# Kernel tuning notes

Hardware: AMD Instinct MI355X
Metric: run time of the kernel (lower is better)

## Reference

```python
import jax, jax.numpy as jnp
import numpy as np

K = 3      # kernel size (fixed by 18 = 2*K*K offset channels)
PAD = 1
EPS = 1e-5 # BatchNorm eps


def setup_inputs() -> dict:
    key = jax.random.key(0)
    ks = jax.random.split(key, 4)
    B, Cin, Cout, H, W = 8, 64, 64, 96, 96
    x = jax.random.normal(ks[0], (B, Cin, H, W), jnp.float32)
    # small offset-conv weights so predicted offsets stay within a few pixels
    w_off = jax.random.normal(ks[1], (2 * K * K, Cin, K, K), jnp.float32) * 0.02
    b_off = jnp.zeros((2 * K * K,), jnp.float32)
    w_def = jax.random.normal(ks[2], (Cout, Cin, K, K), jnp.float32) * (1.0 / np.sqrt(Cin * K * K))
    b_def = jnp.zeros((Cout,), jnp.float32)
    gamma = jnp.ones((Cout,), jnp.float32)
    beta = jnp.zeros((Cout,), jnp.float32)
    return dict(x=x, w_off=w_off, b_off=b_off, w_def=w_def, b_def=b_def, gamma=gamma, beta=beta)


def _deform_sample(x, offset):
    """Bilinear-sample x at deformed kernel tap locations.
    x: (B,C,H,W); offset: (B,2*K*K,H,W) with (dy,dx) pairs per tap, row-major.
    Returns (B,C,K*K,H,W). Out-of-bounds samples are zero (torchvision semantics).
    """
    B, C, H, W = x.shape
    off = offset.reshape(B, K * K, 2, H, W)
    dy, dx = off[:, :, 0], off[:, :, 1]              # (B,9,H,W)
    ky = (jnp.arange(K * K) // K).astype(x.dtype)    # tap row index
    kx = (jnp.arange(K * K) % K).astype(x.dtype)     # tap col index
    base_y = jnp.arange(H, dtype=x.dtype)[:, None] - PAD   # (H,1)
    base_x = jnp.arange(W, dtype=x.dtype)[None, :] - PAD   # (1,W)
    py = dy + ky[None, :, None, None] + base_y[None, None]  # (B,9,H,W)
    px = dx + kx[None, :, None, None] + base_x[None, None]
    y0 = jnp.floor(py)
    x0 = jnp.floor(px)
    wy1 = py - y0
    wx1 = px - x0
    wy0 = 1.0 - wy1
    wx0 = 1.0 - wx1
    xflat = x.reshape(B, C, H * W)
    acc = jnp.zeros((B, C, K * K * H * W), x.dtype)
    corners = [(y0, x0, wy0 * wx0), (y0, x0 + 1.0, wy0 * wx1),
               (y0 + 1.0, x0, wy1 * wx0), (y0 + 1.0, x0 + 1.0, wy1 * wx1)]
    for yc, xc, wc in corners:
        valid = (yc >= 0) & (yc <= H - 1) & (xc >= 0) & (xc <= W - 1)
        iy = jnp.clip(yc, 0, H - 1).astype(jnp.int32)
        ix = jnp.clip(xc, 0, W - 1).astype(jnp.int32)
        idx = (iy * W + ix).reshape(B, 1, K * K * H * W)
        v = jnp.take_along_axis(xflat, idx, axis=2)          # (B,C,9HW) gather
        w = jnp.where(valid, wc, 0.0).reshape(B, 1, K * K * H * W)
        acc = acc + v * w
    return acc.reshape(B, C, K * K, H, W)


def reference(x, w_off, b_off, w_def, b_def, gamma, beta):
    # 1) offset-predicting conv
    offset = jax.lax.conv_general_dilated(
        x, w_off, window_strides=(1, 1), padding=((PAD, PAD), (PAD, PAD)),
        dimension_numbers=("NCHW", "OIHW", "NCHW")) + b_off[None, :, None, None]
    # 2) deformable conv: bilinear gather then per-pixel contraction over (C, taps)
    sampled = _deform_sample(x, offset)                      # (B,C,9,H,W)
    Cout = w_def.shape[0]
    y = jnp.einsum("bckhw,ock->bohw", sampled, w_def.reshape(Cout, -1, K * K))
    y = y + b_def[None, :, None, None]
    # 3) BatchNorm2d (training mode: batch statistics) + ReLU
    mean = y.mean(axis=(0, 2, 3))
    var = y.var(axis=(0, 2, 3))
    y = (y - mean[None, :, None, None]) * jax.lax.rsqrt(var[None, :, None, None] + EPS)
    y = gamma[None, :, None, None] * y + beta[None, :, None, None]
    return jax.nn.relu(y)
```

## Files before the change

### kernel.cpp

```cpp
#include <hip/hip_runtime.h>
#include <hip/hip_bf16.h>
#include <stdint.h>

static constexpr int NBATCH = 8;
static constexpr int Cin  = 64;
static constexpr int Cout = 64;
static constexpr int H = 96, W = 96;
static constexpr int HW   = H * W;
static constexpr int NPIX = NBATCH * HW;
static constexpr int NBLK = NPIX / 64;
static constexpr int BLK_PER_BATCH = HW / 64;
static constexpr float EPS = 1e-5f;

typedef short  bf16x8 __attribute__((ext_vector_type(8)));
typedef float  f32x4  __attribute__((ext_vector_type(4)));

__device__ inline uint16_t f2bf(float f) {
    __hip_bfloat16 h = __float2bfloat16(f);
    return *reinterpret_cast<uint16_t*>(&h);
}
__device__ inline float bf2f(uint16_t u) {
    union { uint32_t i; float f; } z;
    z.i = ((uint32_t)u) << 16;
    return z.f;
}
__device__ inline void gld_lds16(const void* g, void* l) {
    __builtin_amdgcn_global_load_lds(
        (const __attribute__((address_space(1))) void*)g,
        (__attribute__((address_space(3))) void*)l, 16, 0, 0);
}

__global__ void repack(const float* __restrict__ w_off,
                       const float* __restrict__ w_def,
                       uint16_t* __restrict__ woffPack,
                       uint16_t* __restrict__ wdefPack,
                       float* __restrict__ zeropage) {
    int t0 = blockIdx.x * blockDim.x + threadIdx.x;
    int stride = gridDim.x * blockDim.x;
    if (t0 < 64) zeropage[t0] = 0.f;
    for (int i = t0; i < 72 * 32 * 8; i += stride) {
        int e = i & 7;
        int n = (i >> 3) & 31;
        int sg = i >> 8;
        int k = sg * 8 + e;
        int tap = k >> 6, c = k & 63;
        woffPack[i] = (n < 18) ? f2bf(w_off[(n * Cin + c) * 9 + tap]) : (uint16_t)0;
    }
    for (int i = t0; i < 72 * 64 * 8; i += stride) {
        int e = i & 7;
        int n = (i >> 3) & 63;
        int sg = i >> 9;
        int k = sg * 8 + e;
        int tap = k >> 6, c = k & 63;
        wdefPack[i] = f2bf(w_def[(n * Cin + c) * 9 + tap]);
    }
}

__global__ __launch_bounds__(256) void transpose_x(const float* __restrict__ x,
                                                   uint16_t* __restrict__ xT) {
    int t = blockIdx.x * 256 + threadIdx.x;
    int pix  = t >> 1;
    int half = t & 1;
    int b = pix / HW, rem = pix % HW;
    const float* xb = x + (size_t)(b * Cin) * HW + rem + (size_t)(half * 32) * HW;
    uint16_t* o = xT + (size_t)pix * 64 + half * 32;
#pragma unroll
    for (int cg = 0; cg < 4; ++cg) {
        bf16x8 v;
#pragma unroll
        for (int e = 0; e < 8; ++e) v[e] = (short)f2bf(xb[(cg * 8 + e) * HW]);
        *reinterpret_cast<bf16x8*>(o + cg * 8) = v;
    }
}

__global__ __launch_bounds__(512, 4) void fused_deform(
        const uint16_t* __restrict__ xT,
        const uint16_t* __restrict__ woffPack,
        const uint16_t* __restrict__ wdefPack,
        const float* __restrict__ b_off,
        const float* __restrict__ zeropage,
        float* __restrict__ y,
        float* __restrict__ partial) {
    __shared__ __attribute__((aligned(16))) char smem[73728];
    __shared__ float offs[64 * 18];
    __shared__ float s_red[128];
    short* As   = (short*)smem;
    float* osum = (float*)smem;
    float* red  = (float*)smem;

    int tid  = threadIdx.x;
    int lane = tid & 63;
    int wv   = tid >> 6;
    int l15  = lane & 15;
    int lg   = lane >> 4;

    int wgid  = (blockIdx.x & 7) * BLK_PER_BATCH + (blockIdx.x >> 3);
    int gpix0 = wgid * 64;
    int b     = gpix0 / HW;
    int rem0  = gpix0 % HW;
    const uint16_t* xTb = xT + (size_t)b * HW * 64;

    int pr   = (wv << 3) + (lane >> 3);
    int e8   = lane & 7;
    int slot = e8 ^ (pr & 7);
    int remP = rem0 + pr;
    int hP   = remP / W, wP = remP % W;

    {
        const uint16_t* gsrc = xTb + slot * 8;
        char* ldsbase = (char*)As + (size_t)wv * 1024;
#pragma unroll
        for (int tap = 0; tap < 9; ++tap) {
            int yy = hP + tap / 3 - 1;
            int xx = wP + tap % 3 - 1;
            bool ok = (yy >= 0) && (yy < H) && (xx >= 0) && (xx < W);
            const void* g = ok ? (const void*)(gsrc + (yy * W + xx) * 64)
                               : (const void*)zeropage;
            gld_lds16(g, ldsbase + tap * 8192);
        }
    }
    __syncthreads();

    {
        int wj = wv & 1;
        int kq = wv >> 1;
        int sbeg = (kq < 2) ? kq * 5 : 2 + kq * 4;
        int send = (kq < 2) ? sbeg + 5 : sbeg + 4;
        f32x4 oacc[4];
#pragma unroll
        for (int m = 0; m < 4; ++m) oacc[m] = (f32x4){0.f, 0.f, 0.f, 0.f};
        for (int s = sbeg; s < send; ++s) {
            int sg = s * 4 + lg;
            bf16x8 bb = *reinterpret_cast<const bf16x8*>(
                woffPack + (sg * 32 + wj * 16 + l15) * 8);
#pragma unroll
            for (int m = 0; m < 4; ++m) {
                bf16x8 a = *reinterpret_cast<const bf16x8*>(
                    &As[(((sg >> 3) * 64 + m * 16 + l15) * 8 + ((sg & 7) ^ (l15 & 7))) * 8]);
                oacc[m] = __builtin_amdgcn_mfma_f32_16x16x32_bf16(a, bb, oacc[m], 0, 0, 0);
            }
        }
        __syncthreads();
#pragma unroll
        for (int m = 0; m < 4; ++m)
#pragma unroll
            for (int r = 0; r < 4; ++r)
                osum[(kq * 64 + m * 16 + lg * 4 + r) * 34 + wj * 16 + l15] = oacc[m][r];
        __syncthreads();
        for (int i = tid; i < 64 * 18; i += 512) {
            int rr = i / 18, o = i - rr * 18;
            offs[i] = osum[rr * 34 + o] + osum[(64 + rr) * 34 + o]
                    + osum[(128 + rr) * 34 + o] + osum[(192 + rr) * 34 + o] + b_off[o];
        }
        if (tid < 128) s_red[tid] = 0.f;
        __syncthreads();
    }

    {
        float hm1 = (float)(hP - 1), wm1 = (float)(wP - 1);
        float w00a, w01a, w10a, w11a; int i00a, i01a, i10a, i11a;
        {
            int t = e8;
            int ty = (t * 11) >> 5;
            int tx = t - 3 * ty;
            float dy = offs[pr * 18 + 2 * t];
            float dx = offs[pr * 18 + 2 * t + 1];
            float py = dy + (float)ty + hm1;
            float px = dx + (float)tx + wm1;
            float y0f = floorf(py), x0f = floorf(px);
            float wy1 = py - y0f, wx1 = px - x0f;
            float wy0 = 1.f - wy1, wx0 = 1.f - wx1;
            int iy0 = (int)y0f, ix0 = (int)x0f;
            int iy1 = iy0 + 1,  ix1 = ix0 + 1;
            bool vy0 = (iy0 >= 0) && (iy0 < H), vy1 = (iy1 >= 0) && (iy1 < H);
            bool vx0 = (ix0 >= 0) && (ix0 < W), vx1 = (ix1 >= 0) && (ix1 < W);
            w00a = (vy0 && vx0) ? wy0 * wx0 : 0.f;
            w01a = (vy0 && vx1) ? wy0 * wx1 : 0.f;
            w10a = (vy1 && vx0) ? wy1 * wx0 : 0.f;
            w11a = (vy1 && vx1) ? wy1 * wx1 : 0.f;
            int cy0 = min(max(iy0, 0), H - 1), cy1 = min(max(iy1, 0), H - 1);
            int cx0 = min(max(ix0, 0), W - 1), cx1 = min(max(ix1, 0), W - 1);
            i00a = cy0 * W + cx0; i01a = cy0 * W + cx1;
            i10a = cy1 * W + cx0; i11a = cy1 * W + cx1;
        }
        float w00b, w01b, w10b, w11b; int i00b, i01b, i10b, i11b;
        {
            float dy = offs[pr * 18 + 16];
            float dx = offs[pr * 18 + 17];
            float py = dy + 2.f + hm1;
            float px = dx + 2.f + wm1;
            float y0f = floorf(py), x0f = floorf(px);
            float wy1 = py - y0f, wx1 = px - x0f;
            float wy0 = 1.f - wy1, wx0 = 1.f - wx1;
            int iy0 = (int)y0f, ix0 = (int)x0f;
            int iy1 = iy0 + 1,  ix1 = ix0 + 1;
            bool vy0 = (iy0 >= 0) && (iy0 < H), vy1 = (iy1 >= 0) && (iy1 < H);
            bool vx0 = (ix0 >= 0) && (ix0 < W), vx1 = (ix1 >= 0) && (ix1 < W);
            w00b = (vy0 && vx0) ? wy0 * wx0 : 0.f;
            w01b = (vy0 && vx1) ? wy0 * wx1 : 0.f;
            w10b = (vy1 && vx0) ? wy1 * wx0 : 0.f;
            w11b = (vy1 && vx1) ? wy1 * wx1 : 0.f;
            int cy0 = min(max(iy0, 0), H - 1), cy1 = min(max(iy1, 0), H - 1);
            int cx0 = min(max(ix0, 0), W - 1), cx1 = min(max(ix1, 0), W - 1);
            i00b = cy0 * W + cx0; i01b = cy0 * W + cx1;
            i10b = cy1 * W + cx0; i11b = cy1 * W + cx1;
        }

        const uint16_t* basep = xTb + e8 * 8;
        int lanebase = lane & 56;
#pragma unroll
        for (int tap = 0; tap < 9; ++tap) {
            float w00, w01, w10, w11; int i00, i01, i10, i11;
            if (tap < 8) {
                int src = lanebase + tap;
                w00 = __shfl(w00a, src); w01 = __shfl(w01a, src);
                w10 = __shfl(w10a, src); w11 = __shfl(w11a, src);
                i00 = __shfl(i00a, src); i01 = __shfl(i01a, src);
                i10 = __shfl(i10a, src); i11 = __shfl(i11a, src);
            } else {
                w00 = w00b; w01 = w01b; w10 = w10b; w11 = w11b;
                i00 = i00b; i01 = i01b; i10 = i10b; i11 = i11b;
            }
            bf16x8 v00 = *reinterpret_cast<const bf16x8*>(basep + i00 * 64);
            bf16x8 v01 = *reinterpret_cast<const bf16x8*>(basep + i01 * 64);
            bf16x8 v10 = *reinterpret_cast<const bf16x8*>(basep + i10 * 64);
            bf16x8 v11 = *reinterpret_cast<const bf16x8*>(basep + i11 * 64);
            bf16x8 outv;
#pragma unroll
            for (int e = 0; e < 8; ++e) {
                float s = w00 * bf2f((uint16_t)v00[e]) + w01 * bf2f((uint16_t)v01[e])
                        + w10 * bf2f((uint16_t)v10[e]) + w11 * bf2f((uint16_t)v11[e]);
                outv[e] = (short)f2bf(s);
            }
            *reinterpret_cast<bf16x8*>(&As[((tap * 64 + pr) * 8 + slot) * 8]) = outv;
        }
    }
    __syncthreads();

    {
        int nf = wv & 3;
        int kh = wv >> 2;
        f32x4 acc[4];
#pragma unroll
        for (int m = 0; m < 4; ++m) acc[m] = (f32x4){0.f, 0.f, 0.f, 0.f};
#pragma unroll
        for (int s = 0; s < 9; ++s) {
            int sg = (kh * 9 + s) * 4 + lg;
            bf16x8 bb = *reinterpret_cast<const bf16x8*>(
                wdefPack + (sg * 64 + nf * 16 + l15) * 8);
#pragma unroll
            for (int m = 0; m < 4; ++m) {
                bf16x8 a = *reinterpret_cast<const bf16x8*>(
                    &As[(((sg >> 3) * 64 + m * 16 + l15) * 8 + ((sg & 7) ^ (l15 & 7))) * 8]);
                acc[m] = __builtin_amdgcn_mfma_f32_16x16x32_bf16(a, bb, acc[m], 0, 0, 0);
            }
        }
        __syncthreads();
#pragma unroll
        for (int m = 0; m < 4; ++m)
#pragma unroll
            for (int r = 0; r < 4; ++r)
                red[(kh * 64 + m * 16 + lg * 4 + r) * 66 + nf * 16 + l15] = acc[m][r];
        __syncthreads();

        int c  = lane;
        int rg = wv;
        f32x4 v0, v1;
        float s = 0.f, q = 0.f;
#pragma unroll
        for (int k2 = 0; k2 < 8; ++k2) {
            int r = rg * 8 + k2;
            float v = red[r * 66 + c] + red[(64 + r) * 66 + c];
            if (k2 < 4) v0[k2] = v; else v1[k2 - 4] = v;
            s += v; q += v * v;
        }
        float* yp = y + ((size_t)b * Cout + c) * HW + rem0 + rg * 8;
        *reinterpret_cast<f32x4*>(yp)     = v0;
        *reinterpret_cast<f32x4*>(yp + 4) = v1;
        atomicAdd(&s_red[c], s);
        atomicAdd(&s_red[64 + c], q);
    }
    __syncthreads();
    if (tid < 128) partial[(size_t)wgid * 128 + tid] = s_red[tid];
}

__global__ __launch_bounds__(256) void bn_reduce1(const float* __restrict__ partial,
                                                  float* __restrict__ partial2) {
    __shared__ float red[256];
    int ch = threadIdx.x & 127;
    int g  = threadIdx.x >> 7;
    float s = 0.f;
#pragma unroll
    for (int r = 0; r < 8; ++r)
        s += partial[(size_t)(blockIdx.x * 16 + g * 8 + r) * 128 + ch];
    red[threadIdx.x] = s;
    __syncthreads();
    if (g == 0)
        partial2[(size_t)blockIdx.x * 128 + ch] = red[ch] + red[128 + ch];
}

__global__ void bn_stats2(const float* __restrict__ partial2,
                          const float* __restrict__ gamma,
                          const float* __restrict__ beta,
                          float* __restrict__ stats) {
    __shared__ float red[256];
    int ch = threadIdx.x & 127;
    int g  = threadIdx.x >> 7;
    float s = 0.f;
    for (int i = 0; i < 36; ++i)
        s += partial2[(size_t)(g * 36 + i) * 128 + ch];
    red[threadIdx.x] = s;
    __syncthreads();
    if (threadIdx.x < 64) {
        int c = threadIdx.x;
        float sum = red[c] + red[128 + c];
        float sq  = red[64 + c] + red[192 + c];
        float mean = sum / (float)NPIX;
        float var  = sq / (float)NPIX - mean * mean;
        float v    = var + EPS;
        float inv  = rsqrtf(v);
        inv = inv * (1.5f - 0.5f * v * inv * inv);
        float sc = gamma[c] * inv;
        stats[c]      = sc;
        stats[64 + c] = beta[c] - mean * sc;
    }
}

__global__ __launch_bounds__(256) void bn_apply(float* __restrict__ y,
                                                const float* __restrict__ stats) {
    int t = blockIdx.x * blockDim.x + threadIdx.x;
    int e = t * 4;
    int ch = (e / HW) % Cout;
    float sc = stats[ch];
    float sh = stats[64 + ch];
    float4 v = *reinterpret_cast<float4*>(y + e);
    v.x = fmaxf(v.x * sc + sh, 0.f);
    v.y = fmaxf(v.y * sc + sh, 0.f);
    v.z = fmaxf(v.z * sc + sh, 0.f);
    v.w = fmaxf(v.w * sc + sh, 0.f);
    *reinterpret_cast<float4*>(y + e) = v;
}

extern "C" void kernel_launch(void* const* d_in, const int* in_sizes, int n_in,
                              void* d_out, int out_size, void* d_ws, size_t ws_size,
                              hipStream_t stream) {
    const float* x     = (const float*)d_in[0];
    const float* w_off = (const float*)d_in[1];
    const float* b_off = (const float*)d_in[2];
    const float* w_def = (const float*)d_in[3];
    const float* gamma = (const float*)d_in[5];
    const float* beta  = (const float*)d_in[6];
    float* out = (float*)d_out;
    char*  ws  = (char*)d_ws;

    uint16_t* xT       = (uint16_t*)ws;
    uint16_t* woffPack = (uint16_t*)(ws + 9437184);
    uint16_t* wdefPack = (uint16_t*)(ws + 9474048);
    float*    partial  = (float*)(ws + 9547776);
    float*    partial2 = (float*)(ws + 10137600);
    float*    stats    = (float*)(ws + 10174464);
    float*    zeropage = (float*)(ws + 10174976);

    repack<<<64, 256, 0, stream>>>(w_off, w_def, woffPack, wdefPack, zeropage);
    transpose_x<<<NPIX * 2 / 256, 256, 0, stream>>>(x, xT);
    fused_deform<<<NBLK, 512, 0, stream>>>(xT, woffPack, wdefPack, b_off,
                                           zeropage, out, partial);
    bn_reduce1<<<72, 256, 0, stream>>>(partial, partial2);
    bn_stats2<<<1, 256, 0, stream>>>(partial2, gamma, beta, stats);
    bn_apply<<<(NPIX * Cout / 4) / 256, 256, 0, stream>>>(out, stats);
}
```

Before: 67.08 us.

## Shrink LDS footprint by splitting deform taps and reading offset-conv inputs from global

The offset-conv stage now loads its A operands straight from global memory with bounds masking, instead of staging all 9 im2col taps in LDS through global_load_lds. The deformable sampling and MFMA contraction run in two phases (taps 0-3, then 4-8) that reuse a smaller LDS buffer. This cuts shared memory from 72KB to 40KB so the launch bounds can request more resident blocks. The two BN reduction kernels are also merged into a single 1024-thread kernel to save a launch. In exchange, the offset conv makes redundant uncoalesced global/L2 reads, and the extra phase adds barriers.

```diff
diff --git a/kernel.cpp b/kernel.cpp
--- a/kernel.cpp
+++ b/kernel.cpp
@@ -24,20 +24,13 @@
     z.i = ((uint32_t)u) << 16;
     return z.f;
 }
-__device__ inline void gld_lds16(const void* g, void* l) {
-    __builtin_amdgcn_global_load_lds(
-        (const __attribute__((address_space(1))) void*)g,
-        (__attribute__((address_space(3))) void*)l, 16, 0, 0);
-}
 
 __global__ void repack(const float* __restrict__ w_off,
                        const float* __restrict__ w_def,
                        uint16_t* __restrict__ woffPack,
-                       uint16_t* __restrict__ wdefPack,
-                       float* __restrict__ zeropage) {
+                       uint16_t* __restrict__ wdefPack) {
     int t0 = blockIdx.x * blockDim.x + threadIdx.x;
     int stride = gridDim.x * blockDim.x;
-    if (t0 < 64) zeropage[t0] = 0.f;
     for (int i = t0; i < 72 * 32 * 8; i += stride) {
         int e = i & 7;
         int n = (i >> 3) & 31;
@@ -73,15 +66,14 @@
     }
 }
 
-__global__ __launch_bounds__(512, 4) void fused_deform(
+__global__ __launch_bounds__(512, 6) void fused_deform(
         const uint16_t* __restrict__ xT,
         const uint16_t* __restrict__ woffPack,
         const uint16_t* __restrict__ wdefPack,
         const float* __restrict__ b_off,
-        const float* __restrict__ zeropage,
         float* __restrict__ y,
         float* __restrict__ partial) {
-    __shared__ __attribute__((aligned(16))) char smem[73728];
+    __shared__ __attribute__((aligned(16))) char smem[40960];
     __shared__ float offs[64 * 18];
     __shared__ float s_red[128];
     short* As   = (short*)smem;
@@ -106,41 +98,40 @@
     int remP = rem0 + pr;
     int hP   = remP / W, wP = remP % W;
 
-    {
-        const uint16_t* gsrc = xTb + slot * 8;
-        char* ldsbase = (char*)As + (size_t)wv * 1024;
-#pragma unroll
-        for (int tap = 0; tap < 9; ++tap) {
-            int yy = hP + tap / 3 - 1;
-            int xx = wP + tap % 3 - 1;
-            bool ok = (yy >= 0) && (yy < H) && (xx >= 0) && (xx < W);
-            const void* g = ok ? (const void*)(gsrc + (yy * W + xx) * 64)
-                               : (const void*)zeropage;
-            gld_lds16(g, ldsbase + tap * 8192);
-        }
-    }
-    __syncthreads();
+    if (tid < 128) s_red[tid] = 0.f;
 
     {
         int wj = wv & 1;
         int kq = wv >> 1;
         int sbeg = (kq < 2) ? kq * 5 : 2 + kq * 4;
         int send = (kq < 2) ? sbeg + 5 : sbeg + 4;
+        int rm0 = rem0 + l15,      h0_ = rm0 / W, w0_ = rm0 % W;
+        int rm1 = rem0 + 16 + l15, h1_ = rm1 / W, w1_ = rm1 % W;
+        int rm2 = rem0 + 32 + l15, h2_ = rm2 / W, w2_ = rm2 % W;
+        int rm3 = rem0 + 48 + l15, h3_ = rm3 / W, w3_ = rm3 % W;
         f32x4 oacc[4];
 #pragma unroll
         for (int m = 0; m < 4; ++m) oacc[m] = (f32x4){0.f, 0.f, 0.f, 0.f};
         for (int s = sbeg; s < send; ++s) {
-            int sg = s * 4 + lg;
+            int sg  = s * 4 + lg;
+            int tap = s >> 1;
+            int ty  = tap / 3 - 1, tx = tap % 3 - 1;
+            int ch  = (s & 1) * 4 + lg;
             bf16x8 bb = *reinterpret_cast<const bf16x8*>(
                 woffPack + (sg * 32 + wj * 16 + l15) * 8);
 #pragma unroll
             for (int m = 0; m < 4; ++m) {
+                int hh = (m == 0 ? h0_ : m == 1 ? h1_ : m == 2 ? h2_ : h3_) + ty;
+                int ww = (m == 0 ? w0_ : m == 1 ? w1_ : m == 2 ? w2_ : w3_) + tx;
+                bool ok = (hh >= 0) && (hh < H) && (ww >= 0) && (ww < W);
+                int cy = min(max(hh, 0), H - 1);
+                int cx = min(max(ww, 0), W - 1);
                 bf16x8 a = *reinterpret_cast<const bf16x8*>(
-                    &As[(((sg >> 3) * 64 + m * 16 + l15) * 8 + ((sg & 7) ^ (l15 & 7))) * 8]);
+                    xTb + (cy * W + cx) * 64 + ch * 8);
+                if (!ok) a = (bf16x8){0, 0, 0, 0, 0, 0, 0, 0};
                 oacc[m] = __builtin_amdgcn_mfma_f32_16x16x32_bf16(a, bb, oacc[m], 0, 0, 0);
             }
         }
-        __syncthreads();
 #pragma unroll
         for (int m = 0; m < 4; ++m)
 #pragma unroll
@@ -152,117 +143,148 @@
             offs[i] = osum[rr * 34 + o] + osum[(64 + rr) * 34 + o]
                     + osum[(128 + rr) * 34 + o] + osum[(192 + rr) * 34 + o] + b_off[o];
         }
-        if (tid < 128) s_red[tid] = 0.f;
         __syncthreads();
     }
 
+    float hm1 = (float)(hP - 1), wm1 = (float)(wP - 1);
+    float w00a, w01a, w10a, w11a; int i00a, i01a, i10a, i11a;
     {
-        float hm1 = (float)(hP - 1), wm1 = (float)(wP - 1);
-        float w00a, w01a, w10a, w11a; int i00a, i01a, i10a, i11a;
-        {
-            int t = e8;
-            int ty = (t * 11) >> 5;
-            int tx = t - 3 * ty;
-            float dy = offs[pr * 18 + 2 * t];
-            float dx = offs[pr * 18 + 2 * t + 1];
-            float py = dy + (float)ty + hm1;
-            float px = dx + (float)tx + wm1;
-            float y0f = floorf(py), x0f = floorf(px);
-            float wy1 = py - y0f, wx1 = px - x0f;
-            float wy0 = 1.f - wy1, wx0 = 1.f - wx1;
-            int iy0 = (int)y0f, ix0 = (int)x0f;
-            int iy1 = iy0 + 1,  ix1 = ix0 + 1;
-            bool vy0 = (iy0 >= 0) && (iy0 < H), vy1 = (iy1 >= 0) && (iy1 < H);
-            bool vx0 = (ix0 >= 0) && (ix0 < W), vx1 = (ix1 >= 0) && (ix1 < W);
-            w00a = (vy0 && vx0) ? wy0 * wx0 : 0.f;
-            w01a = (vy0 && vx1) ? wy0 * wx1 : 0.f;
-            w10a = (vy1 && vx0) ? wy1 * wx0 : 0.f;
-            w11a = (vy1 && vx1) ? wy1 * wx1 : 0.f;
-            int cy0 = min(max(iy0, 0), H - 1), cy1 = min(max(iy1, 0), H - 1);
-            int cx0 = min(max(ix0, 0), W - 1), cx1 = min(max(ix1, 0), W - 1);
-            i00a = cy0 * W + cx0; i01a = cy0 * W + cx1;
-            i10a = cy1 * W + cx0; i11a = cy1 * W + cx1;
-        }
-        float w00b, w01b, w10b, w11b; int i00b, i01b, i10b, i11b;
-        {
-            float dy = offs[pr * 18 + 16];
-            float dx = offs[pr * 18 + 17];
-            float py = dy + 2.f + hm1;
-            float px = dx + 2.f + wm1;
-            float y0f = floorf(py), x0f = floorf(px);
-            float wy1 = py - y0f, wx1 = px - x0f;
-            float wy0 = 1.f - wy1, wx0 = 1.f - wx1;
-            int iy0 = (int)y0f, ix0 = (int)x0f;
-            int iy1 = iy0 + 1,  ix1 = ix0 + 1;
-            bool vy0 = (iy0 >= 0) && (iy0 < H), vy1 = (iy1 >= 0) && (iy1 < H);
-            bool vx0 = (ix0 >= 0) && (ix0 < W), vx1 = (ix1 >= 0) && (ix1 < W);
-            w00b = (vy0 && vx0) ? wy0 * wx0 : 0.f;
-            w01b = (vy0 && vx1) ? wy0 * wx1 : 0.f;
-            w10b = (vy1 && vx0) ? wy1 * wx0 : 0.f;
-            w11b = (vy1 && vx1) ? wy1 * wx1 : 0.f;
-            int cy0 = min(max(iy0, 0), H - 1), cy1 = min(max(iy1, 0), H - 1);
-            int cx0 = min(max(ix0, 0), W - 1), cx1 = min(max(ix1, 0), W - 1);
-            i00b = cy0 * W + cx0; i01b = cy0 * W + cx1;
-            i10b = cy1 * W + cx0; i11b = cy1 * W + cx1;
-        }
-
-        const uint16_t* basep = xTb + e8 * 8;
-        int lanebase = lane & 56;
-#pragma unroll
-        for (int tap = 0; tap < 9; ++tap) {
-            float w00, w01, w10, w11; int i00, i01, i10, i11;
-            if (tap < 8) {
-                int src = lanebase + tap;
-                w00 = __shfl(w00a, src); w01 = __shfl(w01a, src);
-                w10 = __shfl(w10a, src); w11 = __shfl(w11a, src);
-                i00 = __shfl(i00a, src); i01 = __shfl(i01a, src);
-                i10 = __shfl(i10a, src); i11 = __shfl(i11a, src);
-            } else {
-                w00 = w00b; w01 = w01b; w10 = w10b; w11 = w11b;
-                i00 = i00b; i01 = i01b; i10 = i10b; i11 = i11b;
-            }
-            bf16x8 v00 = *reinterpret_cast<const bf16x8*>(basep + i00 * 64);
-            bf16x8 v01 = *reinterpret_cast<const bf16x8*>(basep + i01 * 64);
-            bf16x8 v10 = *reinterpret_cast<const bf16x8*>(basep + i10 * 64);
-            bf16x8 v11 = *reinterpret_cast<const bf16x8*>(basep + i11 * 64);
-            bf16x8 outv;
-#pragma unroll
-            for (int e = 0; e < 8; ++e) {
-                float s = w00 * bf2f((uint16_t)v00[e]) + w01 * bf2f((uint16_t)v01[e])
-                        + w10 * bf2f((uint16_t)v10[e]) + w11 * bf2f((uint16_t)v11[e]);
-                outv[e] = (short)f2bf(s);
-            }
-            *reinterpret_cast<bf16x8*>(&As[((tap * 64 + pr) * 8 + slot) * 8]) = outv;
-        }
-    }
-    __syncthreads();
-
+        int t = e8;
+        int ty = (t * 11) >> 5;
+        int tx = t - 3 * ty;
+        float dy = offs[pr * 18 + 2 * t];
+        float dx = offs[pr * 18 + 2 * t + 1];
+        float py = dy + (float)ty + hm1;
+        float px = dx + (float)tx + wm1;
+        float y0f = floorf(py), x0f = floorf(px);
+        float wy1 = py - y0f, wx1 = px - x0f;
+        float wy0 = 1.f - wy1, wx0 = 1.f - wx1;
+        int iy0 = (int)y0f, ix0 = (int)x0f;
+        int iy1 = iy0 + 1,  ix1 = ix0 + 1;
+        bool vy0 = (iy0 >= 0) && (iy0 < H), vy1 = (iy1 >= 0) && (iy1 < H);
+        bool vx0 = (ix0 >= 0) && (ix0 < W), vx1 = (ix1 >= 0) && (ix1 < W);
+        w00a = (vy0 && vx0) ? wy0 * wx0 : 0.f;
+        w01a = (vy0 && vx1) ? wy0 * wx1 : 0.f;
+        w10a = (vy1 && vx0) ? wy1 * wx0 : 0.f;
+        w11a = (vy1 && vx1) ? wy1 * wx1 : 0.f;
+        int cy0 = min(max(iy0, 0), H - 1), cy1 = min(max(iy1, 0), H - 1);
+        int cx0 = min(max(ix0, 0), W - 1), cx1 = min(max(ix1, 0), W - 1);
+        i00a = cy0 * W + cx0; i01a = cy0 * W + cx1;
+        i10a = cy1 * W + cx0; i11a = cy1 * W + cx1;
+    }
+    float w00b, w01b, w10b, w11b; int i00b, i01b, i10b, i11b;
     {
-        int nf = wv & 3;
-        int kh = wv >> 2;
-        f32x4 acc[4];
-#pragma unroll
-        for (int m = 0; m < 4; ++m) acc[m] = (f32x4){0.f, 0.f, 0.f, 0.f};
-#pragma unroll
-        for (int s = 0; s < 9; ++s) {
-            int sg = (kh * 9 + s) * 4 + lg;
-            bf16x8 bb = *reinterpret_cast<const bf16x8*>(
-                wdefPack + (sg * 64 + nf * 16 + l15) * 8);
-#pragma unroll
-            for (int m = 0; m < 4; ++m) {
-                bf16x8 a = *reinterpret_cast<const bf16x8*>(
-                    &As[(((sg >> 3) * 64 + m * 16 + l15) * 8 + ((sg & 7) ^ (l15 & 7))) * 8]);
-                acc[m] = __builtin_amdgcn_mfma_f32_16x16x32_bf16(a, bb, acc[m], 0, 0, 0);
-            }
-        }
-        __syncthreads();
-#pragma unroll
-        for (int m = 0; m < 4; ++m)
-#pragma unroll
-            for (int r = 0; r < 4; ++r)
-                red[(kh * 64 + m * 16 + lg * 4 + r) * 66 + nf * 16 + l15] = acc[m][r];
-        __syncthreads();
-
+        float dy = offs[pr * 18 + 16];
+        float dx = offs[pr * 18 + 17];
+        float py = dy + 2.f + hm1;
+        float px = dx + 2.f + wm1;
+        float y0f = floorf(py), x0f = floorf(px);
+        float wy1 = py - y0f, wx1 = px - x0f;
+        float wy0 = 1.f - wy1, wx0 = 1.f - wx1;
+        int iy0 = (int)y0f, ix0 = (int)x0f;
+        int iy1 = iy0 + 1,  ix1 = ix0 + 1;
+        bool vy0 = (iy0 >= 0) && (iy0 < H), vy1 = (iy1 >= 0) && (iy1 < H);
+        bool vx0 = (ix0 >= 0) && (ix0 < W), vx1 = (ix1 >= 0) && (ix1 < W);
+        w00b = (vy0 && vx0) ? wy0 * wx0 : 0.f;
+        w01b = (vy0 && vx1) ? wy0 * wx1 : 0.f;
+        w10b = (vy1 && vx0) ? wy1 * wx0 : 0.f;
+        w11b = (vy1 && vx1) ? wy1 * wx1 : 0.f;
+        int cy0 = min(max(iy0, 0), H - 1), cy1 = min(max(iy1, 0), H - 1);
+        int cx0 = min(max(ix0, 0), W - 1), cx1 = min(max(ix1, 0), W - 1);
+        i00b = cy0 * W + cx0; i01b = cy0 * W + cx1;
+        i10b = cy1 * W + cx0; i11b = cy1 * W + cx1;
+    }
+    const uint16_t* basep = xTb + e8 * 8;
+    int lanebase = lane & 56;
+    int nf = wv & 3;
+    int kh = wv >> 2;
+    f32x4 acc[4];
+#pragma unroll
+    for (int m = 0; m < 4; ++m) acc[m] = (f32x4){0.f, 0.f, 0.f, 0.f};
+
+#pragma unroll
+    for (int tap = 0; tap < 4; ++tap) {
+        int src = lanebase + tap;
+        float w00 = __shfl(w00a, src), w01 = __shfl(w01a, src);
+        float w10 = __shfl(w10a, src), w11 = __shfl(w11a, src);
+        int i00 = __shfl(i00a, src), i01 = __shfl(i01a, src);
+        int i10 = __shfl(i10a, src), i11 = __shfl(i11a, src);
+        bf16x8 v00 = *reinterpret_cast<const bf16x8*>(basep + i00 * 64);
+        bf16x8 v01 = *reinterpret_cast<const bf16x8*>(basep + i01 * 64);
+        bf16x8 v10 = *reinterpret_cast<const bf16x8*>(basep + i10 * 64);
+        bf16x8 v11 = *reinterpret_cast<const bf16x8*>(basep + i11 * 64);
+        bf16x8 outv;
+#pragma unroll
+        for (int e = 0; e < 8; ++e) {
+            float s = w00 * bf2f((uint16_t)v00[e]) + w01 * bf2f((uint16_t)v01[e])
+                    + w10 * bf2f((uint16_t)v10[e]) + w11 * bf2f((uint16_t)v11[e]);
+            outv[e] = (short)f2bf(s);
+        }
+        *reinterpret_cast<bf16x8*>(&As[((tap * 64 + pr) * 8 + slot) * 8]) = outv;
+    }
+    __syncthreads();
+#pragma unroll
+    for (int i = 0; i < 4; ++i) {
+        int sg = kh * 16 + i * 4 + lg;
+        bf16x8 bb = *reinterpret_cast<const bf16x8*>(
+            wdefPack + (sg * 64 + nf * 16 + l15) * 8);
+#pragma unroll
+        for (int m = 0; m < 4; ++m) {
+            bf16x8 a = *reinterpret_cast<const bf16x8*>(
+                &As[(((sg >> 3) * 64 + m * 16 + l15) * 8 + ((sg & 7) ^ (l15 & 7))) * 8]);
+            acc[m] = __builtin_amdgcn_mfma_f32_16x16x32_bf16(a, bb, acc[m], 0, 0, 0);
+        }
+    }
+    __syncthreads();
+
+#pragma unroll
+    for (int tap = 4; tap < 9; ++tap) {
+        float w00, w01, w10, w11; int i00, i01, i10, i11;
+        if (tap < 8) {
+            int src = lanebase + tap;
+            w00 = __shfl(w00a, src); w01 = __shfl(w01a, src);
+            w10 = __shfl(w10a, src); w11 = __shfl(w11a, src);
+            i00 = __shfl(i00a, src); i01 = __shfl(i01a, src);
+            i10 = __shfl(i10a, src); i11 = __shfl(i11a, src);
+        } else {
+            w00 = w00b; w01 = w01b; w10 = w10b; w11 = w11b;
+            i00 = i00b; i01 = i01b; i10 = i10b; i11 = i11b;
+        }
+        bf16x8 v00 = *reinterpret_cast<const bf16x8*>(basep + i00 * 64);
+        bf16x8 v01 = *reinterpret_cast<const bf16x8*>(basep + i01 * 64);
+        bf16x8 v10 = *reinterpret_cast<const bf16x8*>(basep + i10 * 64);
+        bf16x8 v11 = *reinterpret_cast<const bf16x8*>(basep + i11 * 64);
+        bf16x8 outv;
+#pragma unroll
+        for (int e = 0; e < 8; ++e) {
+            float s = w00 * bf2f((uint16_t)v00[e]) + w01 * bf2f((uint16_t)v01[e])
+                    + w10 * bf2f((uint16_t)v10[e]) + w11 * bf2f((uint16_t)v11[e]);
+            outv[e] = (short)f2bf(s);
+        }
+        *reinterpret_cast<bf16x8*>(&As[(((tap - 4) * 64 + pr) * 8 + slot) * 8]) = outv;
+    }
+    __syncthreads();
+#pragma unroll
+    for (int i = 0; i < 5; ++i) {
+        int sgl = kh * 20 + i * 4 + lg;
+        bf16x8 bb = *reinterpret_cast<const bf16x8*>(
+            wdefPack + ((32 + sgl) * 64 + nf * 16 + l15) * 8);
+#pragma unroll
+        for (int m = 0; m < 4; ++m) {
+            bf16x8 a = *reinterpret_cast<const bf16x8*>(
+                &As[(((sgl >> 3) * 64 + m * 16 + l15) * 8 + ((sgl & 7) ^ (l15 & 7))) * 8]);
+            acc[m] = __builtin_amdgcn_mfma_f32_16x16x32_bf16(a, bb, acc[m], 0, 0, 0);
+        }
+    }
+    __syncthreads();
+
+#pragma unroll
+    for (int m = 0; m < 4; ++m)
+#pragma unroll
+        for (int r = 0; r < 4; ++r)
+            red[(kh * 64 + m * 16 + lg * 4 + r) * 66 + nf * 16 + l15] = acc[m][r];
+    __syncthreads();
+    {
         int c  = lane;
         int rg = wv;
         f32x4 v0, v1;
@@ -284,45 +306,34 @@
     if (tid < 128) partial[(size_t)wgid * 128 + tid] = s_red[tid];
 }
 
-__global__ __launch_bounds__(256) void bn_reduce1(const float* __restrict__ partial,
-                                                  float* __restrict__ partial2) {
-    __shared__ float red[256];
-    int ch = threadIdx.x & 127;
-    int g  = threadIdx.x >> 7;
+__global__ __launch_bounds__(1024) void bn_stats(const float* __restrict__ partial,
+                                                 const float* __restrict__ gamma,
+                                                 const float* __restrict__ beta,
+                                                 float* __restrict__ stats) {
+    __shared__ float red[1024];
+    int t = threadIdx.x, ch = t & 127, part = t >> 7;
     float s = 0.f;
-#pragma unroll
-    for (int r = 0; r < 8; ++r)
-        s += partial[(size_t)(blockIdx.x * 16 + g * 8 + r) * 128 + ch];
-    red[threadIdx.x] = s;
-    __syncthreads();
-    if (g == 0)
-        partial2[(size_t)blockIdx.x * 128 + ch] = red[ch] + red[128 + ch];
-}
-
-__global__ void bn_stats2(const float* __restrict__ partial2,
-                          const float* __restrict__ gamma,
-                          const float* __restrict__ beta,
-                          float* __restrict__ stats) {
-    __shared__ float red[256];
-    int ch = threadIdx.x & 127;
-    int g  = threadIdx.x >> 7;
-    float s = 0.f;
-    for (int i = 0; i < 36; ++i)
-        s += partial2[(size_t)(g * 36 + i) * 128 + ch];
-    red[threadIdx.x] = s;
-    __syncthreads();
-    if (threadIdx.x < 64) {
-        int c = threadIdx.x;
-        float sum = red[c] + red[128 + c];
-        float sq  = red[64 + c] + red[192 + c];
+    for (int i = part; i < NBLK; i += 8) s += partial[(size_t)i * 128 + ch];
+    red[t] = s;
+    __syncthreads();
+    if (t < 128) {
+        float a = 0.f;
+#pragma unroll
+        for (int p = 0; p < 8; ++p) a += red[p * 128 + ch];
+        red[t] = a;
+    }
+    __syncthreads();
+    if (t < 64) {
+        float sum = red[t];
+        float sq  = red[64 + t];
         float mean = sum / (float)NPIX;
         float var  = sq / (float)NPIX - mean * mean;
         float v    = var + EPS;
         float inv  = rsqrtf(v);
         inv = inv * (1.5f - 0.5f * v * inv * inv);
-        float sc = gamma[c] * inv;
-        stats[c]      = sc;
-        stats[64 + c] = beta[c] - mean * sc;
+        float sc = gamma[t] * inv;
+        stats[t]      = sc;
+        stats[64 + t] = beta[t] - mean * sc;
     }
 }
 
@@ -357,15 +368,12 @@
     uint16_t* woffPack = (uint16_t*)(ws + 9437184);
     uint16_t* wdefPack = (uint16_t*)(ws + 9474048);
     float*    partial  = (float*)(ws + 9547776);
-    float*    partial2 = (float*)(ws + 10137600);
-    float*    stats    = (float*)(ws + 10174464);
-    float*    zeropage = (float*)(ws + 10174976);
-
-    repack<<<64, 256, 0, stream>>>(w_off, w_def, woffPack, wdefPack, zeropage);
+    float*    stats    = (float*)(ws + 10137600);
+
+    repack<<<64, 256, 0, stream>>>(w_off, w_def, woffPack, wdefPack);
     transpose_x<<<NPIX * 2 / 256, 256, 0, stream>>>(x, xT);
     fused_deform<<<NBLK, 512, 0, stream>>>(xT, woffPack, wdefPack, b_off,
-                                           zeropage, out, partial);
-    bn_reduce1<<<72, 256, 0, stream>>>(partial, partial2);
-    bn_stats2<<<1, 256, 0, stream>>>(partial2, gamma, beta, stats);
+                                           out, partial);
+    bn_stats<<<1, 1024, 0, stream>>>(partial, gamma, beta, stats);
     bn_apply<<<(NPIX * Cout / 4) / 256, 256, 0, stream>>>(out, stats);
 }
```

Result: slower. 111.4 us (+66.0%).
